# Kernel optimization log

Measured on AMD Instinct MI355X. Metric: run time of the kernel, lower is better.

## Reference

```python
import jax, jax.numpy as jnp
import numpy as np

EMBED = 128; HEADS = 4; NUM_CLASSES = 20; NUM_LAYERS = 2
SCENE = (128, 128, 16)
NQ = SCENE[0] * SCENE[1] * SCENE[2]
NI = 300
IMG = (96, 320); ORI = (384, 1280)
VOXEL_SIZE = 0.2
SCORE_THR, MASK_THR, IOU_THR = 0.25, 0.5, 0.8


def _image_grid():
    # generate_grid(image_shape, ori_image_shape), then flip(dims=[0]) -> (x, y) pixel coords in ori resolution
    ys = jnp.arange(IMG[0], dtype=jnp.float32) * (ORI[0] / IMG[0])
    xs = jnp.arange(IMG[1], dtype=jnp.float32) * (ORI[1] / IMG[1])
    gy, gx = jnp.meshgrid(ys, xs, indexing='ij')
    return jnp.stack([gx, gy], 0)  # (2, h, w)


def _scene_pos():
    g = jnp.stack(jnp.meshgrid(*[jnp.arange(s, dtype=jnp.float32) for s in SCENE], indexing='ij'), 0)
    g = (g + 0.5) * VOXEL_SIZE  # project_scale = 1
    return g.reshape(3, -1).T  # (NQ, 3)


def _layernorm(x, g, b):
    mu = x.mean(-1, keepdims=True)
    var = ((x - mu) ** 2).mean(-1, keepdims=True)
    return (x - mu) * jax.lax.rsqrt(var + 1e-5) * g + b


def _mha(q, k, v, w, b):
    # w: (4, D, D) = Wq, Wk, Wv, Wo; b: (4, D)
    B, Nq, D = q.shape; hd = D // HEADS
    def proj(x, i):
        return (x @ w[i].T + b[i]).reshape(B, -1, HEADS, hd).transpose(0, 2, 1, 3)
    qh, kh, vh = proj(q, 0), proj(k, 1), proj(v, 2)
    attn = jax.nn.softmax(jnp.einsum('bhqd,bhkd->bhqk', qh, kh) / jnp.sqrt(jnp.float32(hd)), axis=-1)
    o = jnp.einsum('bhqk,bhkd->bhqd', attn, vh).transpose(0, 2, 1, 3).reshape(B, Nq, D)
    return o @ w[3].T + b[3]


def _tlayer(q, k, v, aw, ab, lg, lb, w1, b1, w2, b2):
    x = _layernorm(q + _mha(q, k, v, aw, ab), lg[0], lb[0])
    h = jax.nn.relu(x @ w1.T + b1) @ w2.T + b2
    return _layernorm(x + h, lg[1], lb[1])


def setup_inputs():
    key = jax.random.key(0)
    ks = jax.random.split(key, 20)
    h, w = IMG
    queries = jax.random.normal(ks[0], (1, NI, EMBED), jnp.float32)
    # 8 instances get a strong class logit so exactly they pass score_thr
    pred_logits = 0.1 * jax.random.normal(ks[1], (1, NI, NUM_CLASSES + 1), jnp.float32)
    ii = jnp.arange(8)
    pred_logits = pred_logits.at[0, ii, ii % (NUM_CLASSES + 1)].add(6.0)
    # each kept instance owns a disjoint 40-px-wide strip -> passes IoU>=0.8
    pred_masks = -6.0 + 0.1 * jax.random.normal(ks[2], (1, NI, h, w), jnp.float32)
    strip = jnp.arange(w) // 40  # 0..7
    boost = 12.0 * (jnp.arange(NI)[:, None] == strip[None, :]).astype(jnp.float32)
    pred_masks = pred_masks + boost[None, :, None, :]
    x3d = 0.1 * jax.random.normal(ks[3], (1, EMBED) + SCENE, jnp.float32)
    depth = 1.0 + 49.0 * jax.random.uniform(ks[4], (1, h, w), jnp.float32)
    K = jnp.array([[[500.0, 0.0, 160.0], [0.0, 500.0, 48.0], [0.0, 0.0, 1.0]]], jnp.float32)
    E = jnp.array([[[1.0, 0.0, 0.0, 0.5], [0.0, 1.0, 0.0, 1.0], [0.0, 0.0, 1.0, 1.5], [0.0, 0.0, 0.0, 1.0]]], jnp.float32)
    voxel_origin = jnp.array([[[0.0, -12.8, -2.0]]], jnp.float32)
    fov_mask = jax.random.bernoulli(ks[5], 0.25, (1, NQ))
    L = NUM_LAYERS
    scene_embed_w = 0.02 * jax.random.normal(ks[6], (NQ, EMBED), jnp.float32)
    inst_pos_w = 0.02 * jax.random.normal(ks[7], (NI, EMBED), jnp.float32)
    pos_w = 0.02 * jax.random.normal(ks[8], (EMBED, 3), jnp.float32)
    conv_w = 0.05 * jax.random.normal(ks[9], (NUM_CLASSES, EMBED), jnp.float32)
    conv_b = jnp.zeros((NUM_CLASSES,), jnp.float32)
    attn_w = 0.05 * jax.random.normal(ks[10], (L, 2, 4, EMBED, EMBED), jnp.float32)
    attn_b = jnp.zeros((L, 2, 4, EMBED), jnp.float32)
    ln_g = jnp.ones((L, 2, 2, EMBED), jnp.float32)
    ln_b = jnp.zeros((L, 2, 2, EMBED), jnp.float32)
    ffn_w1 = 0.05 * jax.random.normal(ks[11], (L, 2, 4 * EMBED, EMBED), jnp.float32)
    ffn_b1 = jnp.zeros((L, 2, 4 * EMBED), jnp.float32)
    ffn_w2 = 0.05 * jax.random.normal(ks[12], (L, 2, EMBED, 4 * EMBED), jnp.float32)
    ffn_b2 = jnp.zeros((L, 2, EMBED), jnp.float32)
    return dict(queries=queries, pred_logits=pred_logits, pred_masks=pred_masks, x3d=x3d, depth=depth,
                K=K, E=E, voxel_origin=voxel_origin, fov_mask=fov_mask,
                scene_embed_w=scene_embed_w, inst_pos_w=inst_pos_w, pos_w=pos_w, conv_w=conv_w, conv_b=conv_b,
                attn_w=attn_w, attn_b=attn_b, ln_g=ln_g, ln_b=ln_b,
                ffn_w1=ffn_w1, ffn_b1=ffn_b1, ffn_w2=ffn_w2, ffn_b2=ffn_b2)


def reference(queries, pred_logits, pred_masks, x3d, depth, K, E, voxel_origin, fov_mask,
              scene_embed_w, inst_pos_w, pos_w, conv_w, conv_b,
              attn_w, attn_b, ln_g, ln_b, ffn_w1, ffn_b1, ffn_w2, ffn_b2):
    h, w = IMG
    # ---- panoptic_postprocess (bs == 1) ----
    sig = jax.nn.sigmoid(pred_logits[0])
    prob_cls = jax.nn.softmax(sig / 0.06, axis=-1)
    scores = prob_cls.max(-1); labels = prob_cls.argmax(-1)
    keep = (labels != prob_cls.shape[-1]) & (scores > SCORE_THR)
    kidx = jnp.nonzero(keep)[0]
    pm = jax.nn.sigmoid(pred_masks[0])[kidx]          # (k, h, w)
    sk = scores[kidx]
    mids = (sk[:, None, None] * pm).argmax(0)          # per-pixel winning instance
    masks = mids[None] == jnp.arange(pm.shape[0])[:, None, None]
    marea = masks.reshape(pm.shape[0], -1).sum(1)
    pmb = pm >= MASK_THR
    parea = pmb.reshape(pm.shape[0], -1).sum(1)
    masks = masks & pmb
    keep_ = (masks.reshape(pm.shape[0], -1).sum(1) > 0) & (marea / parea >= IOU_THR)
    sel = jnp.nonzero(keep_)[0]
    inst_masks = masks[sel]                             # (k2, h, w)
    k2idx = kidx[sel]                                   # final kept slots in [0, NI)
    # ---- gather_mask_pos (depth already at (h, w) -> interpolate is identity) ----
    ig = _image_grid()
    ig3 = jnp.concatenate([ig[None] * depth[:, None], depth[:, None]], axis=1)  # (1,3,h,w) = (x*d, y*d, d)
    cam = jnp.linalg.inv(K) @ ig3.reshape(1, 3, -1)
    homo = jnp.concatenate([cam, jnp.ones((1, 1, h * w), cam.dtype)], axis=1)
    world = (jnp.linalg.inv(E) @ homo)[0, :3].T        # (hw, 3)
    xyz = inst_masks.reshape(inst_masks.shape[0], -1).astype(world.dtype) @ world  # masked sum per instance
    mask_pos = xyz @ pos_w.T                            # Linear(3, embed, bias=False)
    inst_q = queries[0][k2idx][None]                    # (1, k2, D)
    inst_p = (inst_pos_w[k2idx] + mask_pos)[None]
    # ---- scene tokens ----
    scene_embed_full = scene_embed_w[None] + x3d.reshape(1, EMBED, NQ).transpose(0, 2, 1)
    qsrc = scene_embed_full
    fidx = jnp.nonzero(fov_mask[0])[0]
    se = scene_embed_full[:, fidx]
    sp = ((_scene_pos()[None] + voxel_origin)[:, fidx]) @ pos_w.T
    for i in range(NUM_LAYERS):
        inst_q = _tlayer(inst_q + inst_p, se + sp, se, attn_w[i, 0], attn_b[i, 0], ln_g[i, 0], ln_b[i, 0],
                         ffn_w1[i, 0], ffn_b1[i, 0], ffn_w2[i, 0], ffn_b2[i, 0])
        se = _tlayer(se + sp, inst_q + inst_p, inst_q, attn_w[i, 1], attn_b[i, 1], ln_g[i, 1], ln_b[i, 1],
                     ffn_w1[i, 1], ffn_b1[i, 1], ffn_w2[i, 1], ffn_b2[i, 1])
    # ---- index_fov_back_to_voxels + cls_head (project_scale==1 -> Identity + 1x1 Conv3d) ----
    full = qsrc.at[:, fidx].set(se)
    x3d_ = full.transpose(0, 2, 1).reshape(1, EMBED, *SCENE)
    out = jnp.einsum('bcxyz,oc->boxyz', x3d_, conv_w) + conv_b.reshape(1, -1, 1, 1, 1)
    return out
```

## Files before the change

### kernel.cpp

```cpp
#include <hip/hip_runtime.h>
#include <math.h>

#define EMBED 128
#define NCLS 21
#define NI_ 300
#define IMH 96
#define IMW 320
#define NPIX (IMH*IMW)
#define NQ 262144
#define NF_MAX 73728
#define INST_MAX 16
#define IH_MAX 64
#define RS32 0.17677669529663687f

#define S_NF 0
#define S_NK 1
#define S_NINST 2
#define S_NIH 3
#define S_INVK 8
#define S_INVE 24
#define S_KIDX 64
#define S_SKK 400
#define S_MAREA 768
#define S_PAREA 1088
#define S_AREA2 1408
#define S_XYZ 1728
#define S_SELJ 2656
#define S_K2 2688
#define S_FCNT 3072
#define S_FOFF 3328
#define S_INSTQ 4096
#define S_INSTP 6144
#define S_QIN 8192
#define S_QH 10240
#define S_XI 12288
#define S_KHB 16384
#define S_VHB 18432
#define S_QKT 20480
#define S_SB 28672
#define S_SUMV 28928
#define S_WSUM 29056

#define OFF_FIDX ((size_t)1<<20)
#define OFF_INV  ((size_t)2<<20)
#define OFF_W1T  ((size_t)3<<20)
#define OFF_W2T  (((size_t)3<<20) + 512*128*4)
#define OFF_SE   ((size_t)4<<20)
#define SE_BYTES ((size_t)NF_MAX*128*4)
#define OFF_A1   (OFF_SE + SE_BYTES)
#define OFF_A2   (OFF_A1 + SE_BYTES)
#define OFF_SC   (OFF_A2 + SE_BYTES)

__global__ __launch_bounds__(256) void k_init(const float* Km, const float* Em, float* ws){
  int* iw = (int*)ws;
  for (int i = threadIdx.x; i < 4096; i += 256) iw[i] = 0;
  __syncthreads();
  if (threadIdx.x == 0){
    float* fw = ws;
    const float* K = Km;
    float A = K[4]*K[8]-K[5]*K[7];
    float B = K[5]*K[6]-K[3]*K[8];
    float C = K[3]*K[7]-K[4]*K[6];
    float det = K[0]*A + K[1]*B + K[2]*C;
    float id = 1.0f/det;
    fw[S_INVK+0] = A*id;
    fw[S_INVK+1] = (K[2]*K[7]-K[1]*K[8])*id;
    fw[S_INVK+2] = (K[1]*K[5]-K[2]*K[4])*id;
    fw[S_INVK+3] = B*id;
    fw[S_INVK+4] = (K[0]*K[8]-K[2]*K[6])*id;
    fw[S_INVK+5] = (K[2]*K[3]-K[0]*K[5])*id;
    fw[S_INVK+6] = C*id;
    fw[S_INVK+7] = (K[1]*K[6]-K[0]*K[7])*id;
    fw[S_INVK+8] = (K[0]*K[4]-K[1]*K[3])*id;
    float M[4][8];
    for (int r=0;r<4;r++){ for(int c=0;c<4;c++){ M[r][c]=Em[r*4+c]; M[r][4+c]=(r==c)?1.f:0.f; } }
    for (int col=0; col<4; col++){
      int piv=col; float best=fabsf(M[col][col]);
      for (int r=col+1;r<4;r++){ float v=fabsf(M[r][col]); if(v>best){best=v;piv=r;} }
      if (piv!=col){ for(int c=0;c<8;c++){ float tmp=M[col][c]; M[col][c]=M[piv][c]; M[piv][c]=tmp; } }
      float inv=1.0f/M[col][col];
      for (int c=0;c<8;c++) M[col][c]*=inv;
      for (int r=0;r<4;r++){ if(r==col) continue; float f=M[r][col]; for(int c=0;c<8;c++) M[r][c]-=f*M[col][c]; }
    }
    for (int r=0;r<4;r++) for(int c=0;c<4;c++) fw[S_INVE+r*4+c]=M[r][4+c];
  }
}

__global__ __launch_bounds__(320) void k_score(const float* logits, float* ws){
  int* iw=(int*)ws; float* fw=ws;
  __shared__ float ssc[NI_];
  __shared__ int skp[NI_];
  int t=threadIdx.x;
  if (t < NI_){
    float v[NCLS]; float mx=-1e30f;
    for (int c=0;c<NCLS;c++){
      float l=logits[t*NCLS+c];
      float sg=1.0f/(1.0f+expf(-l));
      float x=sg/0.06f;
      v[c]=x; mx=fmaxf(mx,x);
    }
    float s=0.f;
    for (int c=0;c<NCLS;c++) s += expf(v[c]-mx);
    float score=1.0f/s;
    ssc[t]=score; skp[t]=(score>0.25f)?1:0;
  }
  __syncthreads();
  if (t==0){
    int nk=0;
    for (int i=0;i<NI_;i++){ if(skp[i]){ iw[S_KIDX+nk]=i; fw[S_SKK+nk]=ssc[i]; nk++; } }
    iw[S_NK]=nk;
  }
}

__global__ __launch_bounds__(256) void k_winner(const float* pmask, const float* depth, float* ws){
  int* iw=(int*)ws; float* fw=ws;
  int nk=iw[S_NK];
  if (nk>NI_) nk=NI_;
  __shared__ int s_pa[NI_], s_ma[NI_], s_a2[NI_];
  __shared__ float s_x[NI_], s_y[NI_], s_z[NI_];
  __shared__ int s_gi[NI_];
  __shared__ float s_sc[NI_];
  int t=threadIdx.x;
  int lane=t&63;
  for (int j=t;j<nk;j+=256){
    s_pa[j]=0; s_ma[j]=0; s_a2[j]=0;
    s_x[j]=0.f; s_y[j]=0.f; s_z[j]=0.f;
    s_gi[j]=iw[S_KIDX+j]; s_sc[j]=fw[S_SKK+j];
  }
  __syncthreads();
  int p=blockIdx.x*256+t;
  float best=-1e30f; int jw=-1; float mw=0.f;
  for (int j=0;j<nk;j++){
    float m=1.0f/(1.0f+expf(-pmask[(size_t)s_gi[j]*NPIX+p]));
    unsigned long long msk=__ballot(m>=0.5f);
    if (lane==0 && msk) atomicAdd(&s_pa[j], __popcll(msk));
    float wv=s_sc[j]*m;
    if (wv>best){ best=wv; jw=j; mw=m; }
  }
  if (jw>=0){
    atomicAdd(&s_ma[jw],1);
    if (mw>=0.5f){
      atomicAdd(&s_a2[jw],1);
      float d=depth[p];
      float gx=(float)(p%IMW)*4.0f, gy=(float)(p/IMW)*4.0f;
      float X=gx*d, Y=gy*d;
      const float* iK=fw+S_INVK; const float* iE=fw+S_INVE;
      float c0=iK[0]*X+iK[1]*Y+iK[2]*d;
      float c1=iK[3]*X+iK[4]*Y+iK[5]*d;
      float c2=iK[6]*X+iK[7]*Y+iK[8]*d;
      float wx=iE[0]*c0+iE[1]*c1+iE[2]*c2+iE[3];
      float wy=iE[4]*c0+iE[5]*c1+iE[6]*c2+iE[7];
      float wz=iE[8]*c0+iE[9]*c1+iE[10]*c2+iE[11];
      atomicAdd(&s_x[jw],wx);
      atomicAdd(&s_y[jw],wy);
      atomicAdd(&s_z[jw],wz);
    }
  }
  __syncthreads();
  for (int j=t;j<nk;j+=256){
    if (s_pa[j]) atomicAdd(&iw[S_PAREA+j],s_pa[j]);
    if (s_ma[j]) atomicAdd(&iw[S_MAREA+j],s_ma[j]);
    if (s_a2[j]) atomicAdd(&iw[S_AREA2+j],s_a2[j]);
    if (s_x[j]!=0.f) atomicAdd(&fw[S_XYZ+j*3+0],s_x[j]);
    if (s_y[j]!=0.f) atomicAdd(&fw[S_XYZ+j*3+1],s_y[j]);
    if (s_z[j]!=0.f) atomicAdd(&fw[S_XYZ+j*3+2],s_z[j]);
  }
}

__global__ __launch_bounds__(256) void k_sel(const float* queries, const float* instposw, const float* posw, float* ws){
  int* iw=(int*)ws; float* fw=ws;
  __shared__ int sn;
  if (threadIdx.x==0){
    int nk=iw[S_NK]; int n=0;
    for (int j=0;j<nk;j++){
      int a2=iw[S_AREA2+j];
      if (a2>0){
        float r=(float)iw[S_MAREA+j]/(float)iw[S_PAREA+j];
        if (r>=0.8f && n<INST_MAX){ iw[S_SELJ+n]=j; iw[S_K2+n]=iw[S_KIDX+j]; n++; }
      }
    }
    iw[S_NINST]=n; iw[S_NIH]=4*n; sn=n;
  }
  __syncthreads();
  int n=sn;
  for (int idx=threadIdx.x; idx<n*128; idx+=256){
    int i=idx>>7, e=idx&127;
    int j=iw[S_SELJ+i]; int gi=iw[S_K2+i];
    fw[S_INSTQ+idx]=queries[gi*128+e];
    float mp=fw[S_XYZ+j*3]*posw[e*3]+fw[S_XYZ+j*3+1]*posw[e*3+1]+fw[S_XYZ+j*3+2]*posw[e*3+2];
    fw[S_INSTP+idx]=instposw[gi*128+e]+mp;
  }
}

__global__ __launch_bounds__(256) void k_fov_count(const int* fov, float* ws){
  int* iw=(int*)ws;
  __shared__ int red[256];
  int t=threadIdx.x;
  int base=blockIdx.x*1024;
  int s=0;
  for (int k=0;k<4;k++) s += (fov[base+k*256+t]!=0)?1:0;
  red[t]=s; __syncthreads();
  for (int st=128;st>0;st>>=1){ if(t<st) red[t]+=red[t+st]; __syncthreads(); }
  if (t==0) iw[S_FCNT+blockIdx.x]=red[0];
}

__global__ void k_fov_scan(float* ws){
  int* iw=(int*)ws;
  if (threadIdx.x==0){
    int acc=0;
    for (int b=0;b<256;b++){ iw[S_FOFF+b]=acc; acc+=iw[S_FCNT+b]; }
    iw[S_NF]=(acc<NF_MAX)?acc:NF_MAX;
  }
}

__global__ __launch_bounds__(256) void k_fov_scatter(const int* fov, float* ws){
  int* iw=(int*)ws;
  int* fidx=(int*)((char*)ws+OFF_FIDX);
  int* invr=(int*)((char*)ws+OFF_INV);
  __shared__ int wsums[4];
  __shared__ int woff[4];
  __shared__ int cur;
  __shared__ int tot;
  int t=threadIdx.x; int w=t>>6; int lane=t&63;
  if (t==0) cur=iw[S_FOFF+blockIdx.x];
  __syncthreads();
  int base=blockIdx.x*1024;
  for (int k=0;k<4;k++){
    int i=base+k*256+t;
    int f=(fov[i]!=0)?1:0;
    unsigned long long m=__ballot(f);
    int rk=__popcll(m & ((lane==0)?0ull:((~0ull)>>(64-lane))));
    if (lane==0) wsums[w]=__popcll(m);
    __syncthreads();
    if (t==0){ int a=0; for(int q2=0;q2<4;q2++){ woff[q2]=a; a+=wsums[q2]; } tot=a; }
    __syncthreads();
    if (f){
      int r=cur+woff[w]+rk;
      if (r<NF_MAX){ fidx[r]=i; invr[i]=r; } else invr[i]=-1;
    } else invr[i]=-1;
    __syncthreads();
    if (t==0) cur+=tot;
    __syncthreads();
  }
}

__global__ __launch_bounds__(256) void k_se_build(const float* sew, const float* x3d, const int* fidx, float* SE, float* ws){
  int* iw=(int*)ws;
  int nf=iw[S_NF];
  int r0=blockIdx.x*64;
  if (r0>=nf) return;
  int nr=min(64,nf-r0);
  __shared__ float tile[64][129];
  __shared__ int fidxl[64];
  int t=threadIdx.x;
  if (t<64) fidxl[t]=(t<nr)? fidx[r0+t]:0;
  __syncthreads();
  for (int idx=t; idx<64*128; idx+=256){
    int v=idx>>7, e=idx&127;
    tile[v][e]=(v<nr)? sew[(size_t)fidxl[v]*128+e]:0.f;
  }
  __syncthreads();
  for (int idx=t; idx<128*64; idx+=256){
    int c=idx>>6, v=idx&63;
    if (v<nr) tile[v][c]+=x3d[(size_t)c*NQ+fidxl[v]];
  }
  __syncthreads();
  for (int idx=t; idx<64*128; idx+=256){
    int v=idx>>7, e=idx&127;
    if (v<nr) SE[(r0+v)*128+e]=tile[v][e];
  }
}

__global__ __launch_bounds__(256) void kA_prep(const float* Wq, const float* bq, const float* Wk, const float* bk, float* ws){
  int* iw=(int*)ws; float* fw=ws;
  int n=iw[S_NINST]; int nih=iw[S_NIH];
  int t=threadIdx.x;
  for (int idx=t; idx<n*128; idx+=256) fw[S_QIN+idx]=fw[S_INSTQ+idx]+fw[S_INSTP+idx];
  __syncthreads();
  for (int idx=t; idx<n*128; idx+=256){
    int i=idx>>7, e=idx&127;
    float a=bq[e];
    for (int k=0;k<128;k++) a+=fw[S_QIN+i*128+k]*Wq[e*128+k];
    fw[S_QH+idx]=a;
  }
  __syncthreads();
  for (int idx=t; idx<nih*128; idx+=256){
    int ih=idx>>7, e=idx&127;
    int i=ih>>2, h=ih&3;
    float a=0.f;
    for (int d=0;d<32;d++) a+=fw[S_QH+i*128+h*32+d]*Wk[(h*32+d)*128+e];
    fw[S_QKT+idx]=a*RS32;
  }
  for (int ih=t; ih<nih; ih+=256){
    int i=ih>>2, h=ih&3;
    float a=0.f;
    for (int d=0;d<32;d++) a+=fw[S_QH+i*128+h*32+d]*bk[h*32+d];
    fw[S_SB+ih]=a*RS32;
  }
}

__global__ __launch_bounds__(256) void kS1(const float* SE, float* SC, const float* posw, const float* org, const int* fidx, float* ws){
  int* iw=(int*)ws; float* fw=ws;
  int nf=iw[S_NF]; int nih=iw[S_NIH];
  int r0=blockIdx.x*64;
  if (r0>=nf || nih==0) return;
  int nr=min(64,nf-r0);
  __shared__ float xt[64][129];
  __shared__ float qk[IH_MAX*128];
  __shared__ float sbl[IH_MAX];
  __shared__ float pwl[384];
  __shared__ float px[64],py[64],pz[64];
  __shared__ int fidxl[64];
  int t=threadIdx.x;
  for (int i=t;i<384;i+=256) pwl[i]=posw[i];
  if (t<64) fidxl[t]=(t<nr)? fidx[r0+t]:0;
  for (int idx=t; idx<nih*128; idx+=256) qk[idx]=fw[S_QKT+idx];
  if (t<IH_MAX) sbl[t]=(t<nih)? fw[S_SB+t]:0.f;
  __syncthreads();
  if (t<64){
    int q=fidxl[t];
    int vx=q>>11, vy=(q>>4)&127, vz=q&15;
    px[t]=(vx+0.5f)*0.2f+org[0];
    py[t]=(vy+0.5f)*0.2f+org[1];
    pz[t]=(vz+0.5f)*0.2f+org[2];
  }
  __syncthreads();
  for (int idx=t; idx<64*128; idx+=256){
    int v=idx>>7, e=idx&127;
    float val=0.f;
    if (v<nr) val=SE[(r0+v)*128+e]+px[v]*pwl[e*3]+py[v]*pwl[e*3+1]+pz[v]*pwl[e*3+2];
    xt[v][e]=val;
  }
  __syncthreads();
  int tokl=t&63, base=t>>6;
  for (int ih=base; ih<nih; ih+=4){
    float a=sbl[ih];
    const float* qrow=qk+ih*128;
    for (int e=0;e<128;e++) a+=qrow[e]*xt[tokl][e];
    if (tokl<nr) SC[(size_t)ih*NF_MAX+r0+tokl]=a;
  }
}

__global__ __launch_bounds__(256) void kS2S3(float* SC, float* ws){
  int* iw=(int*)ws; float* fw=ws;
  int nih=iw[S_NIH]; int ih=blockIdx.x;
  if (ih>=nih) return;
  int nf=iw[S_NF];
  float* row=SC+(size_t)ih*NF_MAX;
  __shared__ float red[256];
  int t=threadIdx.x;
  float m=-1e30f;
  for (int j=t;j<nf;j+=256) m=fmaxf(m,row[j]);
  red[t]=m; __syncthreads();
  for (int s=128;s>0;s>>=1){ if(t<s) red[t]=fmaxf(red[t],red[t+s]); __syncthreads(); }
  m=red[0]; __syncthreads();
  float sum=0.f;
  for (int j=t;j<nf;j+=256){ float p=expf(row[j]-m); row[j]=p; sum+=p; }
  red[t]=sum; __syncthreads();
  for (int s=128;s>0;s>>=1){ if(t<s) red[t]+=red[t+s]; __syncthreads(); }
  if (t==0) fw[S_SUMV+ih]=red[0];
  if (t<128) fw[S_WSUM+ih*128+t]=0.f;
}

__global__ __launch_bounds__(256) void kS4(const float* SC, const float* SE, float* ws){
  int* iw=(int*)ws; float* fw=ws;
  int nf=iw[S_NF]; int nih=iw[S_NIH];
  if (nih==0) return;
  int t=threadIdx.x;
  int chunk=(nf+255)/256;
  int j0=blockIdx.x*chunk;
  int j1=min(nf,j0+chunk);
  if (j0>=j1) return;
  __shared__ float pt[64*64];
  int e=t&127, half=t>>7;
  float acc[32];
  #pragma unroll
  for (int r=0;r<32;r++) acc[r]=0.f;
  for (int jj=j0; jj<j1; jj+=64){
    int cnt=min(64,j1-jj);
    __syncthreads();
    for (int idx=t; idx<64*64; idx+=256){
      int ih=idx>>6, jl=idx&63;
      pt[idx]=(ih<nih && jl<cnt)? SC[(size_t)ih*NF_MAX+jj+jl]:0.f;
    }
    __syncthreads();
    for (int jl=0; jl<cnt; jl++){
      float sv=SE[(jj+jl)*128+e];
      #pragma unroll
      for (int r=0;r<32;r++) acc[r]+=pt[(half*32+r)*64+jl]*sv;
    }
  }
  #pragma unroll
  for (int r=0;r<32;r++) atomicAdd(&fw[S_WSUM+(half*32+r)*128+e], acc[r]);
}

__global__ __launch_bounds__(256) void kA_post(const float* Wv, const float* bv, const float* Wo, const float* bo,
    const float* g, const float* bb, float* ws){
  int* iw=(int*)ws; float* fw=ws;
  int n=iw[S_NINST]; int nih=iw[S_NIH];
  __shared__ float wn[IH_MAX*128];
  __shared__ float ol[INST_MAX*128];
  __shared__ float tl[INST_MAX*128];
  int t=threadIdx.x;
  for (int idx=t; idx<nih*128; idx+=256){
    int ih=idx>>7;
    wn[idx]=fw[S_WSUM+idx]/fw[S_SUMV+ih];
  }
  __syncthreads();
  for (int idx=t; idx<n*128; idx+=256){
    int i=idx>>7, f=idx&127; int h=f>>5;
    float a=bv[f];
    const float* wrow=Wv+f*128;
    const float* wv=wn+(i*4+h)*128;
    for (int e2=0;e2<128;e2++) a+=wrow[e2]*wv[e2];
    ol[idx]=a;
  }
  __syncthreads();
  for (int idx=t; idx<n*128; idx+=256){
    int i=idx>>7, e2=idx&127;
    float a=bo[e2];
    const float* orow=ol+i*128;
    const float* wrow=Wo+e2*128;
    for (int f2=0;f2<128;f2++) a+=orow[f2]*wrow[f2];
    tl[idx]=a+fw[S_QIN+idx];
  }
  __syncthreads();
  int w=t>>6, lane=t&63;
  for (int i=w;i<n;i+=4){
    float v0=tl[i*128+lane], v1=tl[i*128+64+lane];
    float s=v0+v1;
    for (int o=32;o>0;o>>=1) s+=__shfl_xor(s,o);
    float mu=s*(1.f/128.f);
    float d0=v0-mu, d1=v1-mu;
    float vv=d0*d0+d1*d1;
    for (int o=32;o>0;o>>=1) vv+=__shfl_xor(vv,o);
    float rsv=rsqrtf(vv*(1.f/128.f)+1e-5f);
    fw[S_XI+i*128+lane]=d0*rsv*g[lane]+bb[lane];
    fw[S_XI+i*128+64+lane]=d1*rsv*g[64+lane]+bb[64+lane];
  }
}

__global__ __launch_bounds__(256) void kA_ffn(const float* W1, const float* b1, const float* W2, const float* b2,
    const float* g, const float* bb, float* ws){
  int* iw=(int*)ws; float* fw=ws;
  int n=iw[S_NINST];
  int i=blockIdx.x;
  if (i>=n) return;
  __shared__ float xl[128];
  __shared__ float hid[512];
  __shared__ float yv[128];
  int t=threadIdx.x;
  if (t<128) xl[t]=fw[S_XI+i*128+t];
  __syncthreads();
  for (int d=t; d<512; d+=256){
    float a=b1[d];
    const float* wr=W1+d*128;
    for (int k=0;k<128;k++) a+=wr[k]*xl[k];
    hid[d]=fmaxf(a,0.f);
  }
  __syncthreads();
  if (t<128){
    float a=b2[t];
    const float* wr=W2+(size_t)t*512;
    for (int d=0;d<512;d++) a+=wr[d]*hid[d];
    yv[t]=a+xl[t];
  }
  __syncthreads();
  if (t<64){
    float v0=yv[t], v1=yv[t+64];
    float s=v0+v1;
    for (int o=32;o>0;o>>=1) s+=__shfl_xor(s,o);
    float mu=s*(1.f/128.f);
    float d0=v0-mu, d1=v1-mu;
    float vv=d0*d0+d1*d1;
    for (int o=32;o>0;o>>=1) vv+=__shfl_xor(vv,o);
    float rsv=rsqrtf(vv*(1.f/128.f)+1e-5f);
    fw[S_INSTQ+i*128+t]=d0*rsv*g[t]+bb[t];
    fw[S_INSTQ+i*128+64+t]=d1*rsv*g[64+t]+bb[64+t];
  }
}

__global__ __launch_bounds__(256) void kA_kv(const float* Wk2, const float* bk2, const float* Wv2, const float* bv2, float* ws){
  int* iw=(int*)ws; float* fw=ws;
  int n=iw[S_NINST];
  int t=threadIdx.x;
  for (int idx=t; idx<n*128; idx+=256){
    int i=idx>>7, e=idx&127;
    float ak=bk2[e], av=bv2[e];
    const float* wk=Wk2+e*128;
    const float* wv=Wv2+e*128;
    for (int k=0;k<128;k++){
      float qv=fw[S_INSTQ+i*128+k];
      float qp=qv+fw[S_INSTP+i*128+k];
      ak+=qp*wk[k];
      av+=qv*wv[k];
    }
    fw[S_KHB+idx]=ak; fw[S_VHB+idx]=av;
  }
}

__global__ __launch_bounds__(256) void kGEMM(const float* A, float* C, const float* W, const float* bias,
    int mode_in, int mode_out, const float* SE, const int* fidx,
    const float* posw, const float* org, float* ws){
  int* iw=(int*)ws;
  int nf=iw[S_NF];
  int r0=blockIdx.x*64;
  if (r0>=nf) return;
  int c0=blockIdx.y*64;
  __shared__ float As[64][129];
  __shared__ float Wsh[64][129];
  __shared__ float pwl[384];
  __shared__ float px[64],py[64],pz[64];
  int t=threadIdx.x;
  bool needpos=(mode_in==1)||(mode_out==1);
  if (needpos){
    for (int i=t;i<384;i+=256) pwl[i]=posw[i];
    if (t<64){
      int r=r0+t;
      int q=(r<nf)? fidx[r]:0;
      int vx=q>>11, vy=(q>>4)&127, vz=q&15;
      px[t]=(vx+0.5f)*0.2f+org[0];
      py[t]=(vy+0.5f)*0.2f+org[1];
      pz[t]=(vz+0.5f)*0.2f+org[2];
    }
  }
  __syncthreads();
  for (int idx=t; idx<64*128; idx+=256){
    int rl=idx>>7, k=idx&127;
    int r=r0+rl;
    float v=0.f;
    if (r<nf){
      if (mode_in==1) v=SE[r*128+k]+px[rl]*pwl[k*3]+py[rl]*pwl[k*3+1]+pz[rl]*pwl[k*3+2];
      else v=A[r*128+k];
    }
    As[rl][k]=v;
    Wsh[rl][k]=W[(c0+rl)*128+k];
  }
  __syncthreads();
  int tx=t&15, ty=t>>4;
  float acc[4][4];
  #pragma unroll
  for (int i=0;i<4;i++)
    #pragma unroll
    for (int j=0;j<4;j++) acc[i][j]=0.f;
  #pragma unroll 8
  for (int k=0;k<128;k++){
    float a0=As[ty*4+0][k], a1=As[ty*4+1][k], a2=As[ty*4+2][k], a3=As[ty*4+3][k];
    float w0=Wsh[tx*4+0][k], w1=Wsh[tx*4+1][k], w2=Wsh[tx*4+2][k], w3=Wsh[tx*4+3][k];
    acc[0][0]+=a0*w0; acc[0][1]+=a0*w1; acc[0][2]+=a0*w2; acc[0][3]+=a0*w3;
    acc[1][0]+=a1*w0; acc[1][1]+=a1*w1; acc[1][2]+=a1*w2; acc[1][3]+=a1*w3;
    acc[2][0]+=a2*w0; acc[2][1]+=a2*w1; acc[2][2]+=a2*w2; acc[2][3]+=a2*w3;
    acc[3][0]+=a3*w0; acc[3][1]+=a3*w1; acc[3][2]+=a3*w2; acc[3][3]+=a3*w3;
  }
  for (int i=0;i<4;i++){
    int r=r0+ty*4+i;
    if (r>=nf) continue;
    for (int j=0;j<4;j++){
      int c=c0+tx*4+j;
      float v=acc[i][j]+bias[c];
      if (mode_out==1) v+=SE[r*128+c]+px[ty*4+i]*pwl[c*3]+py[ty*4+i]*pwl[c*3+1]+pz[ty*4+i]*pwl[c*3+2];
      C[r*128+c]=v;
    }
  }
}

__global__ __launch_bounds__(256) void kB2(const float* A1, float* A2, float* ws){
  int* iw=(int*)ws; float* fw=ws;
  int nf=iw[S_NF]; int n=iw[S_NINST];
  int r0=blockIdx.x*64;
  if (r0>=nf) return;
  __shared__ float kh[INST_MAX*128];
  __shared__ float vh[INST_MAX*128];
  __shared__ float ot[64][129];
  int t=threadIdx.x;
  for (int idx=t; idx<INST_MAX*128; idx+=256){
    kh[idx]=(idx<n*128)? fw[S_KHB+idx]:0.f;
    vh[idx]=(idx<n*128)? fw[S_VHB+idx]:0.f;
  }
  __syncthreads();
  int tokl=t&63, h=t>>6;
  int r=r0+tokl;
  bool valid=r<nf;
  float q[32];
  #pragma unroll
  for (int d=0;d<32;d++) q[d]=valid? A1[r*128+h*32+d]:0.f;
  float s[INST_MAX]; float mx=-1e30f;
  for (int j=0;j<INST_MAX;j++){
    float a=0.f;
    #pragma unroll
    for (int d=0;d<32;d++) a+=q[d]*kh[j*128+h*32+d];
    a*=RS32;
    s[j]=(j<n)? a:-1e30f;
    mx=fmaxf(mx,s[j]);
  }
  float sum=0.f;
  for (int j=0;j<INST_MAX;j++){ float p=expf(s[j]-mx); s[j]=p; sum+=p; }
  float inv=(n>0)? 1.0f/sum:0.f;
  float o[32];
  #pragma unroll
  for (int d=0;d<32;d++) o[d]=0.f;
  for (int j=0;j<INST_MAX;j++){
    float a=s[j]*inv;
    #pragma unroll
    for (int d=0;d<32;d++) o[d]+=a*vh[j*128+h*32+d];
  }
  #pragma unroll
  for (int d=0;d<32;d++) ot[tokl][h*32+d]=o[d];
  __syncthreads();
  for (int idx=t; idx<64*128; idx+=256){
    int rl=idx>>7, e=idx&127;
    if (r0+rl<nf) A2[(r0+rl)*128+e]=ot[rl][e];
  }
}

__global__ __launch_bounds__(256) void kLN(const float* A, float* B, const float* g, const float* b, float* ws){
  int* iw=(int*)ws;
  int nf=iw[S_NF];
  int t=threadIdx.x; int w=t>>6; int lane=t&63;
  int r=blockIdx.x*4+w;
  if (r>=nf) return;
  float v0=A[r*128+lane], v1=A[r*128+64+lane];
  float s=v0+v1;
  for (int o=32;o>0;o>>=1) s+=__shfl_xor(s,o);
  float mu=s*(1.0f/128.0f);
  float d0=v0-mu, d1=v1-mu;
  float vv=d0*d0+d1*d1;
  for (int o=32;o>0;o>>=1) vv+=__shfl_xor(vv,o);
  float rsv=rsqrtf(vv*(1.0f/128.0f)+1e-5f);
  B[r*128+lane]=d0*rsv*g[lane]+b[lane];
  B[r*128+64+lane]=d1*rsv*g[64+lane]+b[64+lane];
}

__global__ void k_transpose(const float* in, float* outp, int R, int C){
  __shared__ float tile[32][33];
  int bx=blockIdx.x*32, by=blockIdx.y*32;
  int tx=threadIdx.x, ty=threadIdx.y;
  for (int k=0;k<4;k++){
    int r=by+ty+k*8, c=bx+tx;
    if (r<R && c<C) tile[ty+k*8][tx]=in[(size_t)r*C+c];
  }
  __syncthreads();
  for (int k=0;k<4;k++){
    int cc=bx+ty+k*8, rr=by+tx;
    if (rr<R && cc<C) outp[(size_t)cc*R+rr]=tile[tx][ty+k*8];
  }
}

__global__ __launch_bounds__(256) void kFFN(const float* X_, float* SEo, const float* W1T, const float* W2T,
    const float* b1, const float* b2, const float* g, const float* bb, float* ws){
  int* iw=(int*)ws;
  int nf=iw[S_NF];
  int r0=blockIdx.x*16;
  if (r0>=nf) return;
  __shared__ float X[16][129];
  __shared__ float Hl[16][516];
  __shared__ float yl[16][129];
  int t=threadIdx.x;
  for (int idx=t; idx<16*128; idx+=256){
    int rl=idx>>7, e=idx&127;
    int r=r0+rl;
    X[rl][e]=(r<nf)? X_[r*128+e]:0.f;
  }
  __syncthreads();
  #pragma unroll
  for (int pass=0; pass<2; pass++){
    int d=t+pass*256;
    float acc[16];
    #pragma unroll
    for (int rl=0;rl<16;rl++) acc[rl]=0.f;
    for (int k=0;k<128;k++){
      float w=W1T[k*512+d];
      #pragma unroll
      for (int rl=0;rl<16;rl++) acc[rl]+=w*X[rl][k];
    }
    float bd=b1[d];
    #pragma unroll
    for (int rl=0;rl<16;rl++) Hl[rl][d]=fmaxf(acc[rl]+bd,0.f);
  }
  __syncthreads();
  {
    int e=t&127, g2=t>>7;
    float a2[8];
    #pragma unroll
    for (int rr=0;rr<8;rr++) a2[rr]=0.f;
    for (int d=0;d<512;d++){
      float w=W2T[d*128+e];
      #pragma unroll
      for (int rr=0;rr<8;rr++) a2[rr]+=w*Hl[g2*8+rr][d];
    }
    float be=b2[e];
    #pragma unroll
    for (int rr=0;rr<8;rr++){ int rl=g2*8+rr; yl[rl][e]=a2[rr]+be+X[rl][e]; }
  }
  __syncthreads();
  int w=t>>6, lane=t&63;
  for (int rl=w; rl<16; rl+=4){
    int r=r0+rl;
    float v0=yl[rl][lane], v1=yl[rl][64+lane];
    float s=v0+v1;
    for (int o=32;o>0;o>>=1) s+=__shfl_xor(s,o);
    float mu=s*(1.f/128.f);
    float d0=v0-mu, d1=v1-mu;
    float vv=d0*d0+d1*d1;
    for (int o=32;o>0;o>>=1) vv+=__shfl_xor(vv,o);
    float rsv=rsqrtf(vv*(1.f/128.f)+1e-5f);
    if (r<nf){
      SEo[r*128+lane]=d0*rsv*g[lane]+bb[lane];
      SEo[r*128+64+lane]=d1*rsv*g[64+lane]+bb[64+lane];
    }
  }
}

__global__ __launch_bounds__(256) void k_out(const float* SE, const float* sew, const float* x3d,
    const float* convw, const float* convb, const int* invr, float* out, float* ws){
  (void)ws;
  __shared__ float rows[64][129];
  __shared__ float cw[20*128];
  __shared__ float cb[20];
  __shared__ int rkl[64];
  int t=threadIdx.x;
  int q0=blockIdx.x*64;
  for (int idx=t; idx<20*128; idx+=256) cw[idx]=convw[idx];
  if (t<20) cb[t]=convb[t];
  if (t<64) rkl[t]=invr[q0+t];
  __syncthreads();
  for (int idx=t; idx<64*128; idx+=256){
    int v=idx>>7, e=idx&127;
    int rk=rkl[v];
    rows[v][e]=(rk>=0)? SE[rk*128+e]:sew[(size_t)(q0+v)*128+e];
  }
  __syncthreads();
  for (int idx=t; idx<128*64; idx+=256){
    int c=idx>>6, v=idx&63;
    if (rkl[v]<0) rows[v][c]+=x3d[(size_t)c*NQ+q0+v];
  }
  __syncthreads();
  int v=t&63;
  for (int o=t>>6; o<20; o+=4){
    float a=cb[o];
    const float* cr=cw+o*128;
    for (int c=0;c<128;c++) a+=rows[v][c]*cr[c];
    out[(size_t)o*NQ+q0+v]=a;
  }
}

extern "C" void kernel_launch(void* const* d_in, const int* in_sizes, int n_in,
                              void* d_out, int out_size, void* d_ws, size_t ws_size,
                              hipStream_t stream){
  (void)in_sizes; (void)n_in; (void)out_size; (void)ws_size;
  const float* queries  = (const float*)d_in[0];
  const float* plogits  = (const float*)d_in[1];
  const float* pmasks   = (const float*)d_in[2];
  const float* x3d      = (const float*)d_in[3];
  const float* depth    = (const float*)d_in[4];
  const float* Kmat     = (const float*)d_in[5];
  const float* Emat     = (const float*)d_in[6];
  const float* vorigin  = (const float*)d_in[7];
  const int*   fov      = (const int*)d_in[8];
  const float* sew      = (const float*)d_in[9];
  const float* instposw = (const float*)d_in[10];
  const float* posw     = (const float*)d_in[11];
  const float* convw    = (const float*)d_in[12];
  const float* convb    = (const float*)d_in[13];
  const float* AW       = (const float*)d_in[14];
  const float* AB       = (const float*)d_in[15];
  const float* LG       = (const float*)d_in[16];
  const float* LB       = (const float*)d_in[17];
  const float* F1W      = (const float*)d_in[18];
  const float* F1B      = (const float*)d_in[19];
  const float* F2W      = (const float*)d_in[20];
  const float* F2B      = (const float*)d_in[21];
  float* out = (float*)d_out;
  char* wsb = (char*)d_ws;
  float* fws = (float*)d_ws;
  int* fidx = (int*)(wsb + OFF_FIDX);
  int* invr = (int*)(wsb + OFF_INV);
  float* W1T = (float*)(wsb + OFF_W1T);
  float* W2T = (float*)(wsb + OFF_W2T);
  float* SE = (float*)(wsb + OFF_SE);
  float* A1 = (float*)(wsb + OFF_A1);
  float* A2 = (float*)(wsb + OFF_A2);
  float* SC = (float*)(wsb + OFF_SC);

  auto aw  = [&](int i,int br,int m){ return AW + (size_t)(((i*2+br)*4+m))*128*128; };
  auto ab  = [&](int i,int br,int m){ return AB + (size_t)(((i*2+br)*4+m))*128; };
  auto lng = [&](int i,int br,int wch){ return LG + (size_t)(((i*2+br)*2+wch))*128; };
  auto lnb = [&](int i,int br,int wch){ return LB + (size_t)(((i*2+br)*2+wch))*128; };
  auto f1w = [&](int i,int br){ return F1W + (size_t)(i*2+br)*512*128; };
  auto f1b = [&](int i,int br){ return F1B + (size_t)(i*2+br)*512; };
  auto f2w = [&](int i,int br){ return F2W + (size_t)(i*2+br)*128*512; };
  auto f2b = [&](int i,int br){ return F2B + (size_t)(i*2+br)*128; };

  const int NB64 = NF_MAX/64;
  const int NB16 = NF_MAX/16;
  const int NB4  = NF_MAX/4;

  k_init<<<1,256,0,stream>>>(Kmat,Emat,fws);
  k_score<<<1,320,0,stream>>>(plogits,fws);
  k_winner<<<NPIX/256,256,0,stream>>>(pmasks,depth,fws);
  k_sel<<<1,256,0,stream>>>(queries,instposw,posw,fws);
  k_fov_count<<<256,256,0,stream>>>(fov,fws);
  k_fov_scan<<<1,64,0,stream>>>(fws);
  k_fov_scatter<<<256,256,0,stream>>>(fov,fws);
  k_se_build<<<NB64,256,0,stream>>>(sew,x3d,fidx,SE,fws);

  for (int i=0;i<2;i++){
    kA_prep<<<1,256,0,stream>>>(aw(i,0,0),ab(i,0,0),aw(i,0,1),ab(i,0,1),fws);
    kS1<<<NB64,256,0,stream>>>(SE,SC,posw,vorigin,fidx,fws);
    kS2S3<<<IH_MAX,256,0,stream>>>(SC,fws);
    kS4<<<256,256,0,stream>>>(SC,SE,fws);
    kA_post<<<1,256,0,stream>>>(aw(i,0,2),ab(i,0,2),aw(i,0,3),ab(i,0,3),lng(i,0,0),lnb(i,0,0),fws);
    kA_ffn<<<INST_MAX,256,0,stream>>>(f1w(i,0),f1b(i,0),f2w(i,0),f2b(i,0),lng(i,0,1),lnb(i,0,1),fws);
    kA_kv<<<1,256,0,stream>>>(aw(i,1,1),ab(i,1,1),aw(i,1,2),ab(i,1,2),fws);
    kGEMM<<<dim3(NB64,2),256,0,stream>>>(nullptr,A1,aw(i,1,0),ab(i,1,0),1,0,SE,fidx,posw,vorigin,fws);
    kB2<<<NB64,256,0,stream>>>(A1,A2,fws);
    kGEMM<<<dim3(NB64,2),256,0,stream>>>(A2,A1,aw(i,1,3),ab(i,1,3),0,1,SE,fidx,posw,vorigin,fws);
    kLN<<<NB4,256,0,stream>>>(A1,A2,lng(i,1,0),lnb(i,1,0),fws);
    k_transpose<<<dim3(4,16),dim3(32,8),0,stream>>>(f1w(i,1),W1T,512,128);
    k_transpose<<<dim3(16,4),dim3(32,8),0,stream>>>(f2w(i,1),W2T,128,512);
    kFFN<<<NB16,256,0,stream>>>(A2,SE,W1T,W2T,f1b(i,1),f2b(i,1),lng(i,1,1),lnb(i,1,1),fws);
  }
  k_out<<<NQ/64,256,0,stream>>>(SE,sew,x3d,convw,convb,invr,out,fws);
}
```

Baseline: 2.791 ms.

## Retile scene FFN kernel to 64-row blocks with register-tiled chunked hidden layer

The scene-token FFN kernel now processes 64 rows per block instead of 16, using 4x4 and 4x8 register tiles per thread with float4 loads. The 512-wide hidden layer is computed in 64-column chunks that are consumed immediately by the second GEMM, so the full hidden activation never sits in shared memory. The residual is accumulated in place in the input tile. This raises arithmetic intensity and reuse of each weight load, at the cost of more registers, extra barriers per chunk, and fewer blocks in flight.

```diff
diff --git a/kernel.cpp b/kernel.cpp
--- a/kernel.cpp
+++ b/kernel.cpp
@@ -650,53 +650,101 @@
     const float* b1, const float* b2, const float* g, const float* bb, float* ws){
   int* iw=(int*)ws;
   int nf=iw[S_NF];
-  int r0=blockIdx.x*16;
+  int r0=blockIdx.x*64;
   if (r0>=nf) return;
-  __shared__ float X[16][129];
-  __shared__ float Hl[16][516];
-  __shared__ float yl[16][129];
-  int t=threadIdx.x;
-  for (int idx=t; idx<16*128; idx+=256){
-    int rl=idx>>7, e=idx&127;
+  __shared__ float Xs[64][132];
+  __shared__ float Hs[64][68];
+  int t=threadIdx.x;
+  int tx=t&15, ty=t>>4;
+  int ty4=ty*4;
+  int ecol=tx*8;
+  for (int idx=t; idx<64*32; idx+=256){
+    int rl=idx>>5, e4=idx&31;
     int r=r0+rl;
-    X[rl][e]=(r<nf)? X_[r*128+e]:0.f;
-  }
-  __syncthreads();
+    float4 v = (r<nf)? reinterpret_cast<const float4*>(X_+(size_t)r*128)[e4]
+                     : make_float4(0.f,0.f,0.f,0.f);
+    *reinterpret_cast<float4*>(&Xs[rl][e4*4]) = v;
+  }
+  __syncthreads();
+  float yacc[4][8];
   #pragma unroll
-  for (int pass=0; pass<2; pass++){
-    int d=t+pass*256;
-    float acc[16];
+  for (int i=0;i<4;i++)
     #pragma unroll
-    for (int rl=0;rl<16;rl++) acc[rl]=0.f;
-    for (int k=0;k<128;k++){
-      float w=W1T[k*512+d];
+    for (int j=0;j<8;j++) yacc[i][j]=0.f;
+  for (int dc=0; dc<512; dc+=64){
+    int dcol = dc + tx*4;
+    float acc[4][4];
+    #pragma unroll
+    for (int i=0;i<4;i++)
       #pragma unroll
-      for (int rl=0;rl<16;rl++) acc[rl]+=w*X[rl][k];
-    }
-    float bd=b1[d];
+      for (int j=0;j<4;j++) acc[i][j]=0.f;
+    for (int k=0;k<128;k+=4){
+      float4 w0=*reinterpret_cast<const float4*>(W1T+(size_t)(k+0)*512+dcol);
+      float4 w1=*reinterpret_cast<const float4*>(W1T+(size_t)(k+1)*512+dcol);
+      float4 w2=*reinterpret_cast<const float4*>(W1T+(size_t)(k+2)*512+dcol);
+      float4 w3=*reinterpret_cast<const float4*>(W1T+(size_t)(k+3)*512+dcol);
+      #pragma unroll
+      for (int i=0;i<4;i++){
+        float4 xv=*reinterpret_cast<const float4*>(&Xs[ty4+i][k]);
+        acc[i][0]+=xv.x*w0.x; acc[i][1]+=xv.x*w0.y; acc[i][2]+=xv.x*w0.z; acc[i][3]+=xv.x*w0.w;
+        acc[i][0]+=xv.y*w1.x; acc[i][1]+=xv.y*w1.y; acc[i][2]+=xv.y*w1.z; acc[i][3]+=xv.y*w1.w;
+        acc[i][0]+=xv.z*w2.x; acc[i][1]+=xv.z*w2.y; acc[i][2]+=xv.z*w2.z; acc[i][3]+=xv.z*w2.w;
+        acc[i][0]+=xv.w*w3.x; acc[i][1]+=xv.w*w3.y; acc[i][2]+=xv.w*w3.z; acc[i][3]+=xv.w*w3.w;
+      }
+    }
+    float4 b1v=*reinterpret_cast<const float4*>(b1+dcol);
     #pragma unroll
-    for (int rl=0;rl<16;rl++) Hl[rl][d]=fmaxf(acc[rl]+bd,0.f);
-  }
-  __syncthreads();
-  {
-    int e=t&127, g2=t>>7;
-    float a2[8];
-    #pragma unroll
-    for (int rr=0;rr<8;rr++) a2[rr]=0.f;
-    for (int d=0;d<512;d++){
-      float w=W2T[d*128+e];
+    for (int i=0;i<4;i++){
+      float4 h;
+      h.x=fmaxf(acc[i][0]+b1v.x,0.f);
+      h.y=fmaxf(acc[i][1]+b1v.y,0.f);
+      h.z=fmaxf(acc[i][2]+b1v.z,0.f);
+      h.w=fmaxf(acc[i][3]+b1v.w,0.f);
+      *reinterpret_cast<float4*>(&Hs[ty4+i][tx*4])=h;
+    }
+    __syncthreads();
+    for (int d=0; d<64; d+=4){
+      float4 ha0=*reinterpret_cast<const float4*>(&Hs[ty4+0][d]);
+      float4 ha1=*reinterpret_cast<const float4*>(&Hs[ty4+1][d]);
+      float4 ha2=*reinterpret_cast<const float4*>(&Hs[ty4+2][d]);
+      float4 ha3=*reinterpret_cast<const float4*>(&Hs[ty4+3][d]);
       #pragma unroll
-      for (int rr=0;rr<8;rr++) a2[rr]+=w*Hl[g2*8+rr][d];
-    }
-    float be=b2[e];
-    #pragma unroll
-    for (int rr=0;rr<8;rr++){ int rl=g2*8+rr; yl[rl][e]=a2[rr]+be+X[rl][e]; }
+      for (int kk=0;kk<4;kk++){
+        const float* wrow=W2T+(size_t)(dc+d+kk)*128+ecol;
+        float4 wa=*reinterpret_cast<const float4*>(wrow);
+        float4 wb=*reinterpret_cast<const float4*>(wrow+4);
+        float h0 = (kk==0)?ha0.x:(kk==1)?ha0.y:(kk==2)?ha0.z:ha0.w;
+        float h1 = (kk==0)?ha1.x:(kk==1)?ha1.y:(kk==2)?ha1.z:ha1.w;
+        float h2 = (kk==0)?ha2.x:(kk==1)?ha2.y:(kk==2)?ha2.z:ha2.w;
+        float h3 = (kk==0)?ha3.x:(kk==1)?ha3.y:(kk==2)?ha3.z:ha3.w;
+        yacc[0][0]+=h0*wa.x; yacc[0][1]+=h0*wa.y; yacc[0][2]+=h0*wa.z; yacc[0][3]+=h0*wa.w;
+        yacc[0][4]+=h0*wb.x; yacc[0][5]+=h0*wb.y; yacc[0][6]+=h0*wb.z; yacc[0][7]+=h0*wb.w;
+        yacc[1][0]+=h1*wa.x; yacc[1][1]+=h1*wa.y; yacc[1][2]+=h1*wa.z; yacc[1][3]+=h1*wa.w;
+        yacc[1][4]+=h1*wb.x; yacc[1][5]+=h1*wb.y; yacc[1][6]+=h1*wb.z; yacc[1][7]+=h1*wb.w;
+        yacc[2][0]+=h2*wa.x; yacc[2][1]+=h2*wa.y; yacc[2][2]+=h2*wa.z; yacc[2][3]+=h2*wa.w;
+        yacc[2][4]+=h2*wb.x; yacc[2][5]+=h2*wb.y; yacc[2][6]+=h2*wb.z; yacc[2][7]+=h2*wb.w;
+        yacc[3][0]+=h3*wa.x; yacc[3][1]+=h3*wa.y; yacc[3][2]+=h3*wa.z; yacc[3][3]+=h3*wa.w;
+        yacc[3][4]+=h3*wb.x; yacc[3][5]+=h3*wb.y; yacc[3][6]+=h3*wb.z; yacc[3][7]+=h3*wb.w;
+      }
+    }
+    __syncthreads();
+  }
+  float4 b2a=*reinterpret_cast<const float4*>(b2+ecol);
+  float4 b2b=*reinterpret_cast<const float4*>(b2+ecol+4);
+  #pragma unroll
+  for (int i=0;i<4;i++){
+    float4 xa=*reinterpret_cast<const float4*>(&Xs[ty4+i][ecol]);
+    float4 xb=*reinterpret_cast<const float4*>(&Xs[ty4+i][ecol+4]);
+    xa.x+=yacc[i][0]+b2a.x; xa.y+=yacc[i][1]+b2a.y; xa.z+=yacc[i][2]+b2a.z; xa.w+=yacc[i][3]+b2a.w;
+    xb.x+=yacc[i][4]+b2b.x; xb.y+=yacc[i][5]+b2b.y; xb.z+=yacc[i][6]+b2b.z; xb.w+=yacc[i][7]+b2b.w;
+    *reinterpret_cast<float4*>(&Xs[ty4+i][ecol])=xa;
+    *reinterpret_cast<float4*>(&Xs[ty4+i][ecol+4])=xb;
   }
   __syncthreads();
   int w=t>>6, lane=t&63;
-  for (int rl=w; rl<16; rl+=4){
+  for (int rl=w; rl<64; rl+=4){
     int r=r0+rl;
-    float v0=yl[rl][lane], v1=yl[rl][64+lane];
+    float v0=Xs[rl][lane], v1=Xs[rl][64+lane];
     float s=v0+v1;
     for (int o=32;o>0;o>>=1) s+=__shfl_xor(s,o);
     float mu=s*(1.f/128.f);
@@ -792,7 +840,6 @@
   auto f2b = [&](int i,int br){ return F2B + (size_t)(i*2+br)*128; };
 
   const int NB64 = NF_MAX/64;
-  const int NB16 = NF_MAX/16;
   const int NB4  = NF_MAX/4;
 
   k_init<<<1,256,0,stream>>>(Kmat,Emat,fws);
@@ -818,7 +865,7 @@
     kLN<<<NB4,256,0,stream>>>(A1,A2,lng(i,1,0),lnb(i,1,0),fws);
     k_transpose<<<dim3(4,16),dim3(32,8),0,stream>>>(f1w(i,1),W1T,512,128);
     k_transpose<<<dim3(16,4),dim3(32,8),0,stream>>>(f2w(i,1),W2T,128,512);
-    kFFN<<<NB16,256,0,stream>>>(A2,SE,W1T,W2T,f1b(i,1),f2b(i,1),lng(i,1,1),lnb(i,1,1),fws);
+    kFFN<<<NB64,256,0,stream>>>(A2,SE,W1T,W2T,f1b(i,1),f2b(i,1),lng(i,1,1),lnb(i,1,1),fws);
   }
   k_out<<<NQ/64,256,0,stream>>>(SE,sew,x3d,convw,convb,invr,out,fws);
 }
```

Result: faster. 2.580 ms (-7.6%).
